# Optimization experiments

Measured on AMD Instinct MI355X. Metric: run time of the kernel, lower is better.

## Reference

```python
import jax, jax.numpy as jnp
import numpy as np


def setup_inputs() -> dict:
    key = jax.random.key(0)
    ks = jax.random.split(key, 5)
    B, C, H, W = 16, 512, 64, 64
    cm = cn = C // 4  # int(C*0.5*0.5)
    # kaiming_normal fan_out for 1x1 conv: std = sqrt(2 / out_channels)
    def kaiming(k, out_c, in_c):
        return jax.random.normal(k, (out_c, in_c), jnp.float32) * np.sqrt(2.0 / out_c)
    return {
        "x": jax.random.normal(ks[0], (B, C, H, W), jnp.float32),
        "WA": kaiming(ks[1], cm, C), "bA": jnp.zeros((cm,), jnp.float32),
        "WB": kaiming(ks[2], cn, C), "bB": jnp.zeros((cn,), jnp.float32),
        "WV": kaiming(ks[3], cn, C), "bV": jnp.zeros((cn,), jnp.float32),
        "WR": kaiming(ks[4], C, cm), "bR": jnp.zeros((C,), jnp.float32),
    }


def reference(x, WA, bA, WB, bB, WV, bV, WR, bR):
    b, c, h, w = x.shape
    n = h * w
    xf = x.reshape(b, c, n)  # [b, c, n] flattened spatial
    # 1x1 convs == per-pixel GEMMs
    A = jnp.einsum('mc,bcn->bmn', WA, xf) + bA[None, :, None]          # [b, cm, n]
    Bm = jax.nn.softmax(jnp.einsum('mc,bcn->bmn', WB, xf) + bB[None, :, None], axis=1)  # softmax over channels
    Vm = jax.nn.softmax(jnp.einsum('mc,bcn->bmn', WV, xf) + bV[None, :, None], axis=1)
    # second-order pooling: global descriptors [b, cm, cn]
    gd = jnp.einsum('bmn,bkn->bmk', A, Bm)
    # distribute: [b, cm, n]
    Z = jnp.einsum('bmk,bkn->bmn', gd, Vm)
    # reconstruct 1x1 conv back to c channels
    out = jnp.einsum('cm,bmn->bcn', WR, Z) + bR[None, :, None]
    return out.reshape(b, c, h, w)
```

## Files before the change

### kernel.cpp

```cpp
#include <hip/hip_runtime.h>
#include <hip/hip_fp16.h>


typedef _Float16 half8 __attribute__((ext_vector_type(8)));
typedef float f32x4 __attribute__((ext_vector_type(4)));

__device__ __forceinline__ unsigned short f2h(float v) {
  return __builtin_bit_cast(unsigned short, (_Float16)v);
}

__device__ __forceinline__ f32x4 mfma16(half8 a, half8 b, f32x4 c) {
  return __builtin_amdgcn_mfma_f32_16x16x32_f16(a, b, c, 0, 0, 0);
}

__device__ __forceinline__ int perm32(int v) {
  return (((v & 15) >> 2) << 3) | (((v >> 4) & 1) << 2) | (v & 3);
}

__device__ __forceinline__ void glds16(const unsigned short* g, unsigned short* l) {
  __builtin_amdgcn_global_load_lds(
      (const __attribute__((address_space(1))) unsigned int*)g,
      (__attribute__((address_space(3))) unsigned int*)l, 16, 0, 0);
}

__device__ __forceinline__ void stage_glds(unsigned short* lds,
                                           const unsigned short* g,
                                           int gs, int k0) {
  const int lane = threadIdx.x & 63;
  const int w = threadIdx.x >> 6;
#pragma unroll
  for (int p = 0; p < 2; ++p) {
    int g0 = (w + p * 4) * 64;
    int gi = g0 + lane;
    int row = gi & 127, kg = gi >> 7;
    glds16(g + (size_t)row * gs + k0 + kg * 8, lds + g0 * 8);
  }
}

__device__ __forceinline__ half8 ld_frag(const unsigned short* lds, int row) {
  int kg = (threadIdx.x & 63) >> 4;
  uint4 u = *(const uint4*)&lds[(kg * 128 + row) * 8];
  return __builtin_bit_cast(half8, u);
}

__global__ __launch_bounds__(256) void k_prep_w(
    const float* __restrict__ WA, const float* __restrict__ WB,
    const float* __restrict__ WV, const float* __restrict__ WR,
    unsigned short* __restrict__ Wh, unsigned short* __restrict__ WRh) {
  int idx = blockIdx.x * 256 + threadIdx.x;
  if (idx < 196608) {
    int mg = idx >> 16, r = idx & 65535;
    const float* src = (mg == 0) ? WA : ((mg == 1) ? WB : WV);
    Wh[(idx & ~31) | perm32(idx & 31)] = f2h(src[r]);
  } else {
    int r = idx - 196608;
    WRh[(r & ~31) | perm32(r & 31)] = f2h(WR[r]);
  }
}

__global__ __launch_bounds__(256) void k_transpose_x(
    const float* __restrict__ x, unsigned short* __restrict__ xT) {
  const int n0 = blockIdx.x * 64, c0 = blockIdx.y * 64, b = blockIdx.z;
  __shared__ float sT[64][65];
  const int t = threadIdx.x;
  const int tr = t >> 4, tc4 = (t & 15) * 4;
#pragma unroll
  for (int i = 0; i < 4; ++i) {
    int c = tr + i * 16;
    float4 v = *(const float4*)&x[((size_t)b * 512 + c0 + c) * 4096 + n0 + tc4];
    sT[c][tc4 + 0] = v.x; sT[c][tc4 + 1] = v.y;
    sT[c][tc4 + 2] = v.z; sT[c][tc4 + 3] = v.w;
  }
  __syncthreads();
#pragma unroll
  for (int i = 0; i < 4; ++i) {
    int n = tr + i * 16;
    int cq = tc4;
    ushort4 o;
    o.x = f2h(sT[cq + 0][n]); o.y = f2h(sT[cq + 1][n]);
    o.z = f2h(sT[cq + 2][n]); o.w = f2h(sT[cq + 3][n]);
    int cperm = c0 + (cq & ~31) + perm32(cq & 31);
    *(ushort4*)&xT[((size_t)b * 4096 + n0 + n) * 512 + cperm] = o;
  }
}

__global__ __launch_bounds__(256) void k_gemm_abv(
    const unsigned short* __restrict__ xT, const unsigned short* __restrict__ Wh,
    const float* __restrict__ bA, const float* __restrict__ bB,
    const float* __restrict__ bV,
    unsigned short* __restrict__ Aout, unsigned short* __restrict__ Bmout,
    unsigned short* __restrict__ VmTout) {
  const int nt = blockIdx.x, mg = blockIdx.y, b = blockIdx.z;
  const int tid = threadIdx.x, lane = tid & 63;
  const int w = tid >> 6, wr = w >> 1, wc = w & 1;
  const int kg = lane >> 4, lidx = lane & 15;

  __shared__ unsigned short sW[4096], sX[4096];
  __shared__ float colmax[2][128], colsum[2][128], sBias[128];

  const float* bias = (mg == 0) ? bA : ((mg == 1) ? bB : bV);
  if (tid < 128) sBias[tid] = bias[tid];

  const unsigned short* Wg = Wh + (size_t)mg * 128 * 512;
  const unsigned short* Xg = xT + ((size_t)b * 4096 + (size_t)nt * 128) * 512;

  f32x4 acc[4][4];
#pragma unroll
  for (int mf = 0; mf < 4; ++mf)
#pragma unroll
    for (int nf = 0; nf < 4; ++nf) acc[mf][nf] = (f32x4){0.f, 0.f, 0.f, 0.f};

  for (int k0 = 0; k0 < 512; k0 += 32) {
    stage_glds(sW, Wg, 512, k0);
    stage_glds(sX, Xg, 512, k0);
    __syncthreads();
    half8 af[4];
#pragma unroll
    for (int mf = 0; mf < 4; ++mf) af[mf] = ld_frag(sW, wr * 64 + mf * 16 + lidx);
#pragma unroll
    for (int nf = 0; nf < 4; ++nf) {
      half8 bf = ld_frag(sX, wc * 64 + nf * 16 + lidx);
#pragma unroll
      for (int mf = 0; mf < 4; ++mf) acc[mf][nf] = mfma16(af[mf], bf, acc[mf][nf]);
    }
    __syncthreads();
  }

#pragma unroll
  for (int mf = 0; mf < 4; ++mf)
#pragma unroll
    for (int i = 0; i < 4; ++i) {
      float bb = sBias[wr * 64 + mf * 16 + kg * 4 + i];
#pragma unroll
      for (int nf = 0; nf < 4; ++nf) acc[mf][nf][i] += bb;
    }

  int npg[4];
#pragma unroll
  for (int nf = 0; nf < 4; ++nf) {
    int nin = nf * 16 + lidx;
    npg[nf] = nt * 128 + wc * 64 + (nin & ~31) + perm32(nin & 31);
  }

  const size_t bofs = (size_t)b * 128 * 4096;
  if (mg == 0) {
#pragma unroll
    for (int mf = 0; mf < 4; ++mf)
#pragma unroll
      for (int nf = 0; nf < 4; ++nf)
#pragma unroll
        for (int i = 0; i < 4; ++i) {
          int m_ = wr * 64 + mf * 16 + kg * 4 + i;
          Aout[bofs + (size_t)m_ * 4096 + npg[nf]] = f2h(acc[mf][nf][i]);
        }
    return;
  }

  float cmax[4], csum[4];
#pragma unroll
  for (int nf = 0; nf < 4; ++nf) {
    float m = -1e30f;
#pragma unroll
    for (int mf = 0; mf < 4; ++mf)
#pragma unroll
      for (int i = 0; i < 4; ++i) m = fmaxf(m, acc[mf][nf][i]);
    m = fmaxf(m, __shfl_xor(m, 16));
    m = fmaxf(m, __shfl_xor(m, 32));
    cmax[nf] = m;
  }
  if (kg == 0) {
#pragma unroll
    for (int nf = 0; nf < 4; ++nf) colmax[wr][wc * 64 + nf * 16 + lidx] = cmax[nf];
  }
  __syncthreads();
#pragma unroll
  for (int nf = 0; nf < 4; ++nf)
    cmax[nf] = fmaxf(cmax[nf], colmax[wr ^ 1][wc * 64 + nf * 16 + lidx]);
#pragma unroll
  for (int nf = 0; nf < 4; ++nf) {
    float s = 0.f;
#pragma unroll
    for (int mf = 0; mf < 4; ++mf)
#pragma unroll
      for (int i = 0; i < 4; ++i) {
        float e = __expf(acc[mf][nf][i] - cmax[nf]);
        acc[mf][nf][i] = e;
        s += e;
      }
    s += __shfl_xor(s, 16);
    s += __shfl_xor(s, 32);
    csum[nf] = s;
  }
  if (kg == 0) {
#pragma unroll
    for (int nf = 0; nf < 4; ++nf) colsum[wr][wc * 64 + nf * 16 + lidx] = csum[nf];
  }
  __syncthreads();
  float inv_s[4];
#pragma unroll
  for (int nf = 0; nf < 4; ++nf)
    inv_s[nf] = 1.f / (csum[nf] + colsum[wr ^ 1][wc * 64 + nf * 16 + lidx]);

  if (mg == 1) {
#pragma unroll
    for (int mf = 0; mf < 4; ++mf)
#pragma unroll
      for (int nf = 0; nf < 4; ++nf)
#pragma unroll
        for (int i = 0; i < 4; ++i) {
          int m_ = wr * 64 + mf * 16 + kg * 4 + i;
          Bmout[bofs + (size_t)m_ * 4096 + npg[nf]] = f2h(acc[mf][nf][i] * inv_s[nf]);
        }
  } else {
    const size_t vofs = (size_t)b * 4096 * 128;
#pragma unroll
    for (int mf = 0; mf < 4; ++mf)
#pragma unroll
      for (int nf = 0; nf < 4; ++nf) {
        int m0 = wr * 64 + mf * 16 + kg * 4;
        int mp = (m0 & ~31) + perm32(m0 & 31);
        int n_ = nt * 128 + wc * 64 + nf * 16 + lidx;
        ushort4 pk;
        pk.x = f2h(acc[mf][nf][0] * inv_s[nf]);
        pk.y = f2h(acc[mf][nf][1] * inv_s[nf]);
        pk.z = f2h(acc[mf][nf][2] * inv_s[nf]);
        pk.w = f2h(acc[mf][nf][3] * inv_s[nf]);
        *(ushort4*)&VmTout[vofs + (size_t)n_ * 128 + mp] = pk;
      }
  }
}

__global__ __launch_bounds__(256) void k_gd(
    const unsigned short* __restrict__ A, const unsigned short* __restrict__ Bm,
    float* __restrict__ gd) {
  const int ks = blockIdx.x, b = blockIdx.y;
  const int tid = threadIdx.x, lane = tid & 63;
  const int w = tid >> 6, wr = w >> 1, wc = w & 1;
  const int kg = lane >> 4, lidx = lane & 15;
  __shared__ unsigned short sA[4096], sB[4096];
  const unsigned short* Ab = A + (size_t)b * 128 * 4096 + (size_t)ks * 256;
  const unsigned short* Bb = Bm + (size_t)b * 128 * 4096 + (size_t)ks * 256;

  f32x4 acc[4][4];
#pragma unroll
  for (int mf = 0; mf < 4; ++mf)
#pragma unroll
    for (int nf = 0; nf < 4; ++nf) acc[mf][nf] = (f32x4){0.f, 0.f, 0.f, 0.f};

  for (int k0 = 0; k0 < 256; k0 += 32) {
    stage_glds(sA, Ab, 4096, k0);
    stage_glds(sB, Bb, 4096, k0);
    __syncthreads();
    half8 af[4];
#pragma unroll
    for (int mf = 0; mf < 4; ++mf) af[mf] = ld_frag(sA, wr * 64 + mf * 16 + lidx);
#pragma unroll
    for (int nf = 0; nf < 4; ++nf) {
      half8 bf = ld_frag(sB, wc * 64 + nf * 16 + lidx);
#pragma unroll
      for (int mf = 0; mf < 4; ++mf) acc[mf][nf] = mfma16(af[mf], bf, acc[mf][nf]);
    }
    __syncthreads();
  }
  float* gb = gd + (size_t)b * 128 * 128;
#pragma unroll
  for (int mf = 0; mf < 4; ++mf)
#pragma unroll
    for (int nf = 0; nf < 4; ++nf)
#pragma unroll
      for (int i = 0; i < 4; ++i) {
        int m_ = wr * 64 + mf * 16 + kg * 4 + i;
        int k2 = wc * 64 + nf * 16 + lidx;
        atomicAdd(&gb[(size_t)m_ * 128 + k2], acc[mf][nf][i]);
      }
}

__global__ __launch_bounds__(256) void k_z(
    const float* __restrict__ gd, const unsigned short* __restrict__ VmT,
    unsigned short* __restrict__ ZT) {
  const int nt = blockIdx.x, b = blockIdx.y;
  const int tid = threadIdx.x, lane = tid & 63;
  const int w = tid >> 6, wr = w >> 1, wc = w & 1;
  const int kg = lane >> 4, lidx = lane & 15;
  __shared__ unsigned short sG[4096], sV[4096];
  const float4* gb = (const float4*)(gd + (size_t)b * 128 * 128);
  const unsigned short* Vb = VmT + ((size_t)b * 4096 + (size_t)nt * 128) * 128;

  f32x4 acc[4][4];
#pragma unroll
  for (int mf = 0; mf < 4; ++mf)
#pragma unroll
    for (int nf = 0; nf < 4; ++nf) acc[mf][nf] = (f32x4){0.f, 0.f, 0.f, 0.f};

  for (int k0 = 0; k0 < 128; k0 += 32) {
#pragma unroll
    for (int i = 0; i < 4; ++i) {
      int c = tid + 256 * i;
      int row = c >> 3, q8 = c & 7;
      float4 v = gb[row * 32 + (k0 >> 2) + q8];
      unsigned int lo = (unsigned)f2h(v.x) | ((unsigned)f2h(v.y) << 16);
      unsigned int hi = (unsigned)f2h(v.z) | ((unsigned)f2h(v.w) << 16);
      int kgq = q8 & 3, h = q8 >> 2;
      *(uint2*)&sG[(kgq * 128 + row) * 8 + h * 4] = make_uint2(lo, hi);
    }
    stage_glds(sV, Vb, 128, k0);
    __syncthreads();
    half8 af[4];
#pragma unroll
    for (int mf = 0; mf < 4; ++mf) af[mf] = ld_frag(sG, wr * 64 + mf * 16 + lidx);
#pragma unroll
    for (int nf = 0; nf < 4; ++nf) {
      half8 bf = ld_frag(sV, wc * 64 + nf * 16 + lidx);
#pragma unroll
      for (int mf = 0; mf < 4; ++mf) acc[mf][nf] = mfma16(af[mf], bf, acc[mf][nf]);
    }
    __syncthreads();
  }
  const size_t zofs = (size_t)b * 4096 * 128;
#pragma unroll
  for (int mf = 0; mf < 4; ++mf)
#pragma unroll
    for (int nf = 0; nf < 4; ++nf) {
      int m0 = wr * 64 + mf * 16 + kg * 4;
      int mp = (m0 & ~31) + perm32(m0 & 31);
      int n_ = nt * 128 + wc * 64 + nf * 16 + lidx;
      ushort4 pk;
      pk.x = f2h(acc[mf][nf][0]);
      pk.y = f2h(acc[mf][nf][1]);
      pk.z = f2h(acc[mf][nf][2]);
      pk.w = f2h(acc[mf][nf][3]);
      *(ushort4*)&ZT[zofs + (size_t)n_ * 128 + mp] = pk;
    }
}

__global__ __launch_bounds__(256) void k_out(
    const unsigned short* __restrict__ WRh, const unsigned short* __restrict__ ZT,
    const float* __restrict__ bR, float* __restrict__ out) {
  const int nt = blockIdx.x, ct = blockIdx.y, b = blockIdx.z;
  const int tid = threadIdx.x, lane = tid & 63;
  const int w = tid >> 6, wr = w >> 1, wc = w & 1;
  const int kg = lane >> 4, lidx = lane & 15;
  __shared__ unsigned short sW[4096], sZ[4096];
  __shared__ float sBias[128];
  if (tid < 128) sBias[tid] = bR[ct * 128 + tid];
  const unsigned short* Wb = WRh + (size_t)ct * 128 * 128;
  const unsigned short* Zb = ZT + ((size_t)b * 4096 + (size_t)nt * 128) * 128;

  f32x4 acc[4][4];
#pragma unroll
  for (int mf = 0; mf < 4; ++mf)
#pragma unroll
    for (int nf = 0; nf < 4; ++nf) acc[mf][nf] = (f32x4){0.f, 0.f, 0.f, 0.f};

  for (int k0 = 0; k0 < 128; k0 += 32) {
    stage_glds(sW, Wb, 128, k0);
    stage_glds(sZ, Zb, 128, k0);
    __syncthreads();
    half8 af[4];
#pragma unroll
    for (int mf = 0; mf < 4; ++mf) af[mf] = ld_frag(sW, wr * 64 + mf * 16 + lidx);
#pragma unroll
    for (int nf = 0; nf < 4; ++nf) {
      half8 bf = ld_frag(sZ, wc * 64 + nf * 16 + lidx);
#pragma unroll
      for (int mf = 0; mf < 4; ++mf) acc[mf][nf] = mfma16(af[mf], bf, acc[mf][nf]);
    }
    __syncthreads();
  }
#pragma unroll
  for (int mf = 0; mf < 4; ++mf)
#pragma unroll
    for (int nf = 0; nf < 4; ++nf)
#pragma unroll
      for (int i = 0; i < 4; ++i) {
        int cl = wr * 64 + mf * 16 + kg * 4 + i;
        int n_ = nt * 128 + wc * 64 + nf * 16 + lidx;
        out[((size_t)b * 512 + ct * 128 + cl) * 4096 + n_] = acc[mf][nf][i] + sBias[cl];
      }
}

extern "C" void kernel_launch(void* const* d_in, const int* in_sizes, int n_in,
                              void* d_out, int out_size, void* d_ws, size_t ws_size,
                              hipStream_t stream) {
  const float* x  = (const float*)d_in[0];
  const float* WA = (const float*)d_in[1];
  const float* bA = (const float*)d_in[2];
  const float* WB = (const float*)d_in[3];
  const float* bB = (const float*)d_in[4];
  const float* WV = (const float*)d_in[5];
  const float* bV = (const float*)d_in[6];
  const float* WR = (const float*)d_in[7];
  const float* bR = (const float*)d_in[8];
  float* out = (float*)d_out;

  char* ws = (char*)d_ws;
  unsigned short* Wh   = (unsigned short*)(ws);
  unsigned short* WRh  = (unsigned short*)(ws + 393216);
  unsigned short* xT   = (unsigned short*)(ws + 524288);
  unsigned short* Aout = (unsigned short*)(ws + 67633152);
  unsigned short* Bm   = (unsigned short*)(ws + 84410368);
  unsigned short* VmT  = (unsigned short*)(ws + 101187584);
  float*          gd   = (float*)(ws + 117964800);
  unsigned short* ZT   = (unsigned short*)(ws + 119013376);

  hipMemsetAsync(gd, 0, (size_t)16 * 128 * 128 * sizeof(float), stream);
  k_prep_w<<<1024, 256, 0, stream>>>(WA, WB, WV, WR, Wh, WRh);
  k_transpose_x<<<dim3(64, 8, 16), 256, 0, stream>>>(x, xT);
  k_gemm_abv<<<dim3(32, 3, 16), 256, 0, stream>>>(xT, Wh, bA, bB, bV, Aout, Bm, VmT);
  k_gd<<<dim3(16, 16), 256, 0, stream>>>(Aout, Bm, gd);
  k_z<<<dim3(32, 16), 256, 0, stream>>>(gd, VmT, ZT);
  k_out<<<dim3(32, 4, 16), 256, 0, stream>>>(WRh, ZT, bR, out);
}
```

Before: 184.0 us.

## Fuse x transpose, ABV GEMM and gd pooling; fold WR into gd

Removes the separate fp32→fp16 transpose of x: the fused kernel reads x directly, converts it in registers and double-buffers x and W tiles in shared memory. All three projections (A, Bm, Vm) are computed in one 384-thread block. A and Bm stay in LDS and their per-tile contribution to gd is accumulated with atomics, so the large A/Bm intermediates are never written to global memory. Reassociation multiplies WR by gd per batch (k_gw), which removes the Z pass and lets k_out consume Vm directly. The trade-offs are fewer blocks (512) with heavy LDS use, and an added fp16 rounding on the combined WR·gd weights.

```diff
diff --git a/kernel.cpp b/kernel.cpp
--- a/kernel.cpp
+++ b/kernel.cpp
@@ -8,24 +8,29 @@
 __device__ __forceinline__ unsigned short f2h(float v) {
   return __builtin_bit_cast(unsigned short, (_Float16)v);
 }
-
+__device__ __forceinline__ unsigned pk2(float a, float b) {
+  return (unsigned)f2h(a) | ((unsigned)f2h(b) << 16);
+}
 __device__ __forceinline__ f32x4 mfma16(half8 a, half8 b, f32x4 c) {
   return __builtin_amdgcn_mfma_f32_16x16x32_f16(a, b, c, 0, 0, 0);
 }
-
 __device__ __forceinline__ int perm32(int v) {
   return (((v & 15) >> 2) << 3) | (((v >> 4) & 1) << 2) | (v & 3);
 }
-
 __device__ __forceinline__ void glds16(const unsigned short* g, unsigned short* l) {
   __builtin_amdgcn_global_load_lds(
       (const __attribute__((address_space(1))) unsigned int*)g,
       (__attribute__((address_space(3))) unsigned int*)l, 16, 0, 0);
 }
-
-__device__ __forceinline__ void stage_glds(unsigned short* lds,
-                                           const unsigned short* g,
-                                           int gs, int k0) {
+__device__ __forceinline__ half8 ld_frag(const unsigned short* lds, int row) {
+  int kg = (threadIdx.x & 63) >> 4;
+  uint4 u = *(const uint4*)&lds[(kg * 128 + row) * 8];
+  return __builtin_bit_cast(half8, u);
+}
+
+__device__ __forceinline__ void stage_glds256(unsigned short* lds,
+                                              const unsigned short* g,
+                                              int gs, int k0) {
   const int lane = threadIdx.x & 63;
   const int w = threadIdx.x >> 6;
 #pragma unroll
@@ -37,209 +42,246 @@
   }
 }
 
-__device__ __forceinline__ half8 ld_frag(const unsigned short* lds, int row) {
-  int kg = (threadIdx.x & 63) >> 4;
-  uint4 u = *(const uint4*)&lds[(kg * 128 + row) * 8];
-  return __builtin_bit_cast(half8, u);
-}
-
-__global__ __launch_bounds__(256) void k_prep_w(
+__global__ __launch_bounds__(256) void k_prep(
     const float* __restrict__ WA, const float* __restrict__ WB,
     const float* __restrict__ WV, const float* __restrict__ WR,
-    unsigned short* __restrict__ Wh, unsigned short* __restrict__ WRh) {
+    unsigned short* __restrict__ Wh, unsigned short* __restrict__ WRh,
+    float* __restrict__ gdT) {
   int idx = blockIdx.x * 256 + threadIdx.x;
   if (idx < 196608) {
     int mg = idx >> 16, r = idx & 65535;
     const float* src = (mg == 0) ? WA : ((mg == 1) ? WB : WV);
     Wh[(idx & ~31) | perm32(idx & 31)] = f2h(src[r]);
-  } else {
+  } else if (idx < 262144) {
     int r = idx - 196608;
     WRh[(r & ~31) | perm32(r & 31)] = f2h(WR[r]);
-  }
-}
-
-__global__ __launch_bounds__(256) void k_transpose_x(
-    const float* __restrict__ x, unsigned short* __restrict__ xT) {
-  const int n0 = blockIdx.x * 64, c0 = blockIdx.y * 64, b = blockIdx.z;
-  __shared__ float sT[64][65];
-  const int t = threadIdx.x;
-  const int tr = t >> 4, tc4 = (t & 15) * 4;
-#pragma unroll
-  for (int i = 0; i < 4; ++i) {
-    int c = tr + i * 16;
-    float4 v = *(const float4*)&x[((size_t)b * 512 + c0 + c) * 4096 + n0 + tc4];
-    sT[c][tc4 + 0] = v.x; sT[c][tc4 + 1] = v.y;
-    sT[c][tc4 + 2] = v.z; sT[c][tc4 + 3] = v.w;
-  }
-  __syncthreads();
-#pragma unroll
-  for (int i = 0; i < 4; ++i) {
-    int n = tr + i * 16;
-    int cq = tc4;
-    ushort4 o;
-    o.x = f2h(sT[cq + 0][n]); o.y = f2h(sT[cq + 1][n]);
-    o.z = f2h(sT[cq + 2][n]); o.w = f2h(sT[cq + 3][n]);
-    int cperm = c0 + (cq & ~31) + perm32(cq & 31);
-    *(ushort4*)&xT[((size_t)b * 4096 + n0 + n) * 512 + cperm] = o;
-  }
-}
-
-__global__ __launch_bounds__(256) void k_gemm_abv(
-    const unsigned short* __restrict__ xT, const unsigned short* __restrict__ Wh,
+  } else {
+    gdT[idx - 262144] = 0.f;
+  }
+}
+
+__global__ __launch_bounds__(384) void k_abv_gd(
+    const float* __restrict__ x, const unsigned short* __restrict__ Wh,
     const float* __restrict__ bA, const float* __restrict__ bB,
     const float* __restrict__ bV,
-    unsigned short* __restrict__ Aout, unsigned short* __restrict__ Bmout,
-    unsigned short* __restrict__ VmTout) {
-  const int nt = blockIdx.x, mg = blockIdx.y, b = blockIdx.z;
-  const int tid = threadIdx.x, lane = tid & 63;
-  const int w = tid >> 6, wr = w >> 1, wc = w & 1;
+    unsigned short* __restrict__ VmT, float* __restrict__ gdT) {
+  const int nt = blockIdx.x, b = blockIdx.y;
+  const int tid = threadIdx.x, lane = tid & 63, w = tid >> 6;
   const int kg = lane >> 4, lidx = lane & 15;
-
-  __shared__ unsigned short sW[4096], sX[4096];
-  __shared__ float colmax[2][128], colsum[2][128], sBias[128];
-
-  const float* bias = (mg == 0) ? bA : ((mg == 1) ? bB : bV);
-  if (tid < 128) sBias[tid] = bias[tid];
-
-  const unsigned short* Wg = Wh + (size_t)mg * 128 * 512;
-  const unsigned short* Xg = xT + ((size_t)b * 4096 + (size_t)nt * 128) * 512;
-
-  f32x4 acc[4][4];
+  const int mg = w >> 1, wh = w & 1;
+
+  __shared__ unsigned short smem[32768];
+  __shared__ float cmaxs[2][2][128], csums[2][2][128];
+  __shared__ float sBias[384];
+
+  sBias[tid] = ((mg == 0) ? bA : ((mg == 1) ? bB : bV))[tid & 127];
+
+  const float* xbase = x + (size_t)b * 512 * 4096 + nt * 128;
+  const int xn = tid & 127;
+  const int xkg = tid >> 7;
+  const bool x2 = (tid >= 256);
+
+  float xr[16];
+
+#define XLOAD(K0) do { \
+  _Pragma("unroll") for (int j = 0; j < 4; ++j) { \
+    xr[j]     = xbase[(size_t)((K0) + 4 * xkg + j) * 4096 + xn]; \
+    xr[4 + j] = xbase[(size_t)((K0) + 16 + 4 * xkg + j) * 4096 + xn]; \
+  } \
+  if (x2) { _Pragma("unroll") for (int j = 0; j < 4; ++j) { \
+    xr[8 + j]  = xbase[(size_t)((K0) + 12 + j) * 4096 + xn]; \
+    xr[12 + j] = xbase[(size_t)((K0) + 28 + j) * 4096 + xn]; \
+  } } } while (0)
+
+#define XWRITE(SX) do { \
+  uint4 u_; \
+  u_.x = pk2(xr[0], xr[1]); u_.y = pk2(xr[2], xr[3]); \
+  u_.z = pk2(xr[4], xr[5]); u_.w = pk2(xr[6], xr[7]); \
+  *(uint4*)&(SX)[(xkg * 128 + xn) * 8] = u_; \
+  if (x2) { \
+    uint4 v_; \
+    v_.x = pk2(xr[8], xr[9]);   v_.y = pk2(xr[10], xr[11]); \
+    v_.z = pk2(xr[12], xr[13]); v_.w = pk2(xr[14], xr[15]); \
+    *(uint4*)&(SX)[(3 * 128 + xn) * 8] = v_; \
+  } } while (0)
+
+#define WSTAGE(SW, K0) do { \
+  _Pragma("unroll") for (int p = 0; p < 4; ++p) { \
+    int g0_ = (w * 4 + p) * 64; \
+    int gi_ = g0_ + lane; \
+    int mgt_ = gi_ >> 9, q_ = gi_ & 511; \
+    int kgw_ = q_ >> 7, row_ = q_ & 127; \
+    glds16(Wh + mgt_ * 65536 + row_ * 512 + (K0) + kgw_ * 8, (SW) + g0_ * 8); \
+  } } while (0)
+
+  f32x4 acc[4][8];
 #pragma unroll
   for (int mf = 0; mf < 4; ++mf)
 #pragma unroll
-    for (int nf = 0; nf < 4; ++nf) acc[mf][nf] = (f32x4){0.f, 0.f, 0.f, 0.f};
-
-  for (int k0 = 0; k0 < 512; k0 += 32) {
-    stage_glds(sW, Wg, 512, k0);
-    stage_glds(sX, Xg, 512, k0);
+    for (int nf = 0; nf < 8; ++nf) acc[mf][nf] = (f32x4){0.f, 0.f, 0.f, 0.f};
+
+  XLOAD(0);
+  WSTAGE(smem, 0);
+  XWRITE(smem + 12288);
+
+  for (int ks = 0; ks < 16; ++ks) {
+    unsigned short* cw = smem + (ks & 1) * 16384;
+    unsigned short* nx = smem + ((ks & 1) ^ 1) * 16384;
     __syncthreads();
+    if (ks < 15) {
+      XLOAD((ks + 1) * 32);
+      WSTAGE(nx, (ks + 1) * 32);
+    }
     half8 af[4];
 #pragma unroll
-    for (int mf = 0; mf < 4; ++mf) af[mf] = ld_frag(sW, wr * 64 + mf * 16 + lidx);
-#pragma unroll
-    for (int nf = 0; nf < 4; ++nf) {
-      half8 bf = ld_frag(sX, wc * 64 + nf * 16 + lidx);
-#pragma unroll
-      for (int mf = 0; mf < 4; ++mf) acc[mf][nf] = mfma16(af[mf], bf, acc[mf][nf]);
-    }
-    __syncthreads();
+    for (int mf = 0; mf < 4; ++mf)
+      af[mf] = ld_frag(cw + mg * 4096, wh * 64 + mf * 16 + lidx);
+#pragma unroll
+    for (int nf = 0; nf < 8; ++nf) {
+      half8 bf = ld_frag(cw + 12288, nf * 16 + lidx);
+#pragma unroll
+      for (int mf = 0; mf < 4; ++mf)
+        acc[mf][nf] = mfma16(af[mf], bf, acc[mf][nf]);
+    }
+    if (ks < 15) XWRITE(nx + 12288);
   }
 
 #pragma unroll
   for (int mf = 0; mf < 4; ++mf)
 #pragma unroll
     for (int i = 0; i < 4; ++i) {
-      float bb = sBias[wr * 64 + mf * 16 + kg * 4 + i];
-#pragma unroll
-      for (int nf = 0; nf < 4; ++nf) acc[mf][nf][i] += bb;
-    }
-
-  int npg[4];
-#pragma unroll
-  for (int nf = 0; nf < 4; ++nf) {
-    int nin = nf * 16 + lidx;
-    npg[nf] = nt * 128 + wc * 64 + (nin & ~31) + perm32(nin & 31);
-  }
-
-  const size_t bofs = (size_t)b * 128 * 4096;
-  if (mg == 0) {
+      float bb = sBias[mg * 128 + wh * 64 + mf * 16 + kg * 4 + i];
+#pragma unroll
+      for (int nf = 0; nf < 8; ++nf) acc[mf][nf][i] += bb;
+    }
+
+  float inv_s[8];
+  if (mg) {
+#pragma unroll
+    for (int nf = 0; nf < 8; ++nf) {
+      float m = -1e30f;
+#pragma unroll
+      for (int mf = 0; mf < 4; ++mf)
+#pragma unroll
+        for (int i = 0; i < 4; ++i) m = fmaxf(m, acc[mf][nf][i]);
+      m = fmaxf(m, __shfl_xor(m, 16));
+      m = fmaxf(m, __shfl_xor(m, 32));
+      if (kg == 0) cmaxs[mg - 1][wh][nf * 16 + lidx] = m;
+      inv_s[nf] = m;
+    }
+  }
+  __syncthreads();
+  if (mg) {
+#pragma unroll
+    for (int nf = 0; nf < 8; ++nf) {
+      float m = fmaxf(inv_s[nf], cmaxs[mg - 1][wh ^ 1][nf * 16 + lidx]);
+      float s = 0.f;
+#pragma unroll
+      for (int mf = 0; mf < 4; ++mf)
+#pragma unroll
+        for (int i = 0; i < 4; ++i) {
+          float e = __expf(acc[mf][nf][i] - m);
+          acc[mf][nf][i] = e;
+          s += e;
+        }
+      s += __shfl_xor(s, 16);
+      s += __shfl_xor(s, 32);
+      if (kg == 0) csums[mg - 1][wh][nf * 16 + lidx] = s;
+      inv_s[nf] = s;
+    }
+  }
+  __syncthreads();
+  if (mg) {
+#pragma unroll
+    for (int nf = 0; nf < 8; ++nf)
+      inv_s[nf] = 1.f / (inv_s[nf] + csums[mg - 1][wh ^ 1][nf * 16 + lidx]);
+  }
+
+  unsigned short* sA2 = smem;
+  unsigned short* sB2 = smem + 16384;
+
+  if (mg != 2) {
+    unsigned short* dst = (mg == 0) ? sA2 : sB2;
+#pragma unroll
+    for (int nf = 0; nf < 8; ++nf) {
+      int base = (nf >> 1) * 4096 + (lidx >> 2) * 1024 + (nf & 1) * 4 + (lidx & 3);
+#pragma unroll
+      for (int mf = 0; mf < 4; ++mf)
+#pragma unroll
+        for (int i = 0; i < 4; ++i) {
+          int m_ = wh * 64 + mf * 16 + kg * 4 + i;
+          float v = acc[mf][nf][i];
+          dst[base + m_ * 8] = f2h(mg ? v * inv_s[nf] : v);
+        }
+    }
+  }
+  __syncthreads();
+
+  if (mg != 2) {
+    const int gr = wh, gc = mg;
+    f32x4 g2[4][4];
 #pragma unroll
     for (int mf = 0; mf < 4; ++mf)
 #pragma unroll
+      for (int nf = 0; nf < 4; ++nf) g2[mf][nf] = (f32x4){0.f, 0.f, 0.f, 0.f};
+#pragma unroll
+    for (int ks2 = 0; ks2 < 4; ++ks2) {
+      half8 af2[4];
+#pragma unroll
+      for (int mf = 0; mf < 4; ++mf)
+        af2[mf] = ld_frag(sA2 + ks2 * 4096, gr * 64 + mf * 16 + lidx);
+#pragma unroll
+      for (int nf = 0; nf < 4; ++nf) {
+        half8 bf2 = ld_frag(sB2 + ks2 * 4096, gc * 64 + nf * 16 + lidx);
+#pragma unroll
+        for (int mf = 0; mf < 4; ++mf)
+          g2[mf][nf] = mfma16(af2[mf], bf2, g2[mf][nf]);
+      }
+    }
+    float* gb = gdT + (size_t)b * 16384;
+#pragma unroll
+    for (int mf = 0; mf < 4; ++mf)
+#pragma unroll
       for (int nf = 0; nf < 4; ++nf)
 #pragma unroll
         for (int i = 0; i < 4; ++i) {
-          int m_ = wr * 64 + mf * 16 + kg * 4 + i;
-          Aout[bofs + (size_t)m_ * 4096 + npg[nf]] = f2h(acc[mf][nf][i]);
-        }
-    return;
-  }
-
-  float cmax[4], csum[4];
-#pragma unroll
-  for (int nf = 0; nf < 4; ++nf) {
-    float m = -1e30f;
-#pragma unroll
-    for (int mf = 0; mf < 4; ++mf)
-#pragma unroll
-      for (int i = 0; i < 4; ++i) m = fmaxf(m, acc[mf][nf][i]);
-    m = fmaxf(m, __shfl_xor(m, 16));
-    m = fmaxf(m, __shfl_xor(m, 32));
-    cmax[nf] = m;
-  }
-  if (kg == 0) {
-#pragma unroll
-    for (int nf = 0; nf < 4; ++nf) colmax[wr][wc * 64 + nf * 16 + lidx] = cmax[nf];
-  }
-  __syncthreads();
-#pragma unroll
-  for (int nf = 0; nf < 4; ++nf)
-    cmax[nf] = fmaxf(cmax[nf], colmax[wr ^ 1][wc * 64 + nf * 16 + lidx]);
-#pragma unroll
-  for (int nf = 0; nf < 4; ++nf) {
-    float s = 0.f;
-#pragma unroll
-    for (int mf = 0; mf < 4; ++mf)
-#pragma unroll
-      for (int i = 0; i < 4; ++i) {
-        float e = __expf(acc[mf][nf][i] - cmax[nf]);
-        acc[mf][nf][i] = e;
-        s += e;
-      }
-    s += __shfl_xor(s, 16);
-    s += __shfl_xor(s, 32);
-    csum[nf] = s;
-  }
-  if (kg == 0) {
-#pragma unroll
-    for (int nf = 0; nf < 4; ++nf) colsum[wr][wc * 64 + nf * 16 + lidx] = csum[nf];
-  }
-  __syncthreads();
-  float inv_s[4];
-#pragma unroll
-  for (int nf = 0; nf < 4; ++nf)
-    inv_s[nf] = 1.f / (csum[nf] + colsum[wr ^ 1][wc * 64 + nf * 16 + lidx]);
-
-  if (mg == 1) {
-#pragma unroll
-    for (int mf = 0; mf < 4; ++mf)
-#pragma unroll
-      for (int nf = 0; nf < 4; ++nf)
-#pragma unroll
-        for (int i = 0; i < 4; ++i) {
-          int m_ = wr * 64 + mf * 16 + kg * 4 + i;
-          Bmout[bofs + (size_t)m_ * 4096 + npg[nf]] = f2h(acc[mf][nf][i] * inv_s[nf]);
+          int m_ = gr * 64 + mf * 16 + kg * 4 + i;
+          int k2 = gc * 64 + nf * 16 + lidx;
+          atomicAdd(&gb[k2 * 128 + m_], g2[mf][nf][i]);
         }
   } else {
-    const size_t vofs = (size_t)b * 4096 * 128;
-#pragma unroll
-    for (int mf = 0; mf < 4; ++mf)
-#pragma unroll
-      for (int nf = 0; nf < 4; ++nf) {
-        int m0 = wr * 64 + mf * 16 + kg * 4;
-        int mp = (m0 & ~31) + perm32(m0 & 31);
-        int n_ = nt * 128 + wc * 64 + nf * 16 + lidx;
+    const size_t vofs = ((size_t)b * 4096 + (size_t)nt * 128) * 128;
+#pragma unroll
+    for (int mf = 0; mf < 4; ++mf) {
+      int m0 = wh * 64 + mf * 16 + kg * 4;
+      int mp = (m0 & ~31) + perm32(m0 & 31);
+#pragma unroll
+      for (int nf = 0; nf < 8; ++nf) {
+        int n_ = nf * 16 + lidx;
         ushort4 pk;
         pk.x = f2h(acc[mf][nf][0] * inv_s[nf]);
         pk.y = f2h(acc[mf][nf][1] * inv_s[nf]);
         pk.z = f2h(acc[mf][nf][2] * inv_s[nf]);
         pk.w = f2h(acc[mf][nf][3] * inv_s[nf]);
-        *(ushort4*)&VmTout[vofs + (size_t)n_ * 128 + mp] = pk;
+        *(ushort4*)&VmT[vofs + (size_t)n_ * 128 + mp] = pk;
       }
-  }
-}
-
-__global__ __launch_bounds__(256) void k_gd(
-    const unsigned short* __restrict__ A, const unsigned short* __restrict__ Bm,
-    float* __restrict__ gd) {
-  const int ks = blockIdx.x, b = blockIdx.y;
+    }
+  }
+#undef XLOAD
+#undef XWRITE
+#undef WSTAGE
+}
+
+__global__ __launch_bounds__(256) void k_gw(
+    const float* __restrict__ gdT, const unsigned short* __restrict__ WRh,
+    unsigned short* __restrict__ GWh) {
+  const int ct = blockIdx.x, b = blockIdx.y;
   const int tid = threadIdx.x, lane = tid & 63;
   const int w = tid >> 6, wr = w >> 1, wc = w & 1;
   const int kg = lane >> 4, lidx = lane & 15;
-  __shared__ unsigned short sA[4096], sB[4096];
-  const unsigned short* Ab = A + (size_t)b * 128 * 4096 + (size_t)ks * 256;
-  const unsigned short* Bb = Bm + (size_t)b * 128 * 4096 + (size_t)ks * 256;
+  __shared__ unsigned short sG[4096], sWr[4096];
+  const float* gb = gdT + (size_t)b * 16384;
+  const unsigned short* Wb = WRh + ct * 128 * 128;
 
   f32x4 acc[4][4];
 #pragma unroll
@@ -247,94 +289,50 @@
 #pragma unroll
     for (int nf = 0; nf < 4; ++nf) acc[mf][nf] = (f32x4){0.f, 0.f, 0.f, 0.f};
 
-  for (int k0 = 0; k0 < 256; k0 += 32) {
-    stage_glds(sA, Ab, 4096, k0);
-    stage_glds(sB, Bb, 4096, k0);
+  for (int k0 = 0; k0 < 128; k0 += 32) {
+#pragma unroll
+    for (int p = 0; p < 2; ++p) {
+      int g = tid + p * 256;
+      int row = g & 127, kgx = g >> 7;
+      const float* s0 = &gb[row * 128 + k0 + 4 * kgx];
+      float4 v0 = *(const float4*)s0;
+      float4 v1 = *(const float4*)(s0 + 16);
+      uint4 u;
+      u.x = pk2(v0.x, v0.y); u.y = pk2(v0.z, v0.w);
+      u.z = pk2(v1.x, v1.y); u.w = pk2(v1.z, v1.w);
+      *(uint4*)&sG[g * 8] = u;
+    }
+    stage_glds256(sWr, Wb, 128, k0);
     __syncthreads();
     half8 af[4];
 #pragma unroll
-    for (int mf = 0; mf < 4; ++mf) af[mf] = ld_frag(sA, wr * 64 + mf * 16 + lidx);
+    for (int mf = 0; mf < 4; ++mf) af[mf] = ld_frag(sG, wr * 64 + mf * 16 + lidx);
 #pragma unroll
     for (int nf = 0; nf < 4; ++nf) {
-      half8 bf = ld_frag(sB, wc * 64 + nf * 16 + lidx);
+      half8 bf = ld_frag(sWr, wc * 64 + nf * 16 + lidx);
 #pragma unroll
       for (int mf = 0; mf < 4; ++mf) acc[mf][nf] = mfma16(af[mf], bf, acc[mf][nf]);
     }
     __syncthreads();
   }
-  float* gb = gd + (size_t)b * 128 * 128;
-#pragma unroll
-  for (int mf = 0; mf < 4; ++mf)
-#pragma unroll
-    for (int nf = 0; nf < 4; ++nf)
-#pragma unroll
-      for (int i = 0; i < 4; ++i) {
-        int m_ = wr * 64 + mf * 16 + kg * 4 + i;
-        int k2 = wc * 64 + nf * 16 + lidx;
-        atomicAdd(&gb[(size_t)m_ * 128 + k2], acc[mf][nf][i]);
-      }
-}
-
-__global__ __launch_bounds__(256) void k_z(
-    const float* __restrict__ gd, const unsigned short* __restrict__ VmT,
-    unsigned short* __restrict__ ZT) {
-  const int nt = blockIdx.x, b = blockIdx.y;
-  const int tid = threadIdx.x, lane = tid & 63;
-  const int w = tid >> 6, wr = w >> 1, wc = w & 1;
-  const int kg = lane >> 4, lidx = lane & 15;
-  __shared__ unsigned short sG[4096], sV[4096];
-  const float4* gb = (const float4*)(gd + (size_t)b * 128 * 128);
-  const unsigned short* Vb = VmT + ((size_t)b * 4096 + (size_t)nt * 128) * 128;
-
-  f32x4 acc[4][4];
-#pragma unroll
-  for (int mf = 0; mf < 4; ++mf)
-#pragma unroll
-    for (int nf = 0; nf < 4; ++nf) acc[mf][nf] = (f32x4){0.f, 0.f, 0.f, 0.f};
-
-  for (int k0 = 0; k0 < 128; k0 += 32) {
-#pragma unroll
-    for (int i = 0; i < 4; ++i) {
-      int c = tid + 256 * i;
-      int row = c >> 3, q8 = c & 7;
-      float4 v = gb[row * 32 + (k0 >> 2) + q8];
-      unsigned int lo = (unsigned)f2h(v.x) | ((unsigned)f2h(v.y) << 16);
-      unsigned int hi = (unsigned)f2h(v.z) | ((unsigned)f2h(v.w) << 16);
-      int kgq = q8 & 3, h = q8 >> 2;
-      *(uint2*)&sG[(kgq * 128 + row) * 8 + h * 4] = make_uint2(lo, hi);
-    }
-    stage_glds(sV, Vb, 128, k0);
-    __syncthreads();
-    half8 af[4];
-#pragma unroll
-    for (int mf = 0; mf < 4; ++mf) af[mf] = ld_frag(sG, wr * 64 + mf * 16 + lidx);
+  const size_t gofs = ((size_t)b * 512 + (size_t)ct * 128) * 128;
+#pragma unroll
+  for (int mf = 0; mf < 4; ++mf) {
+    int k0g = wr * 64 + mf * 16 + kg * 4;
+    int kp = (k0g & ~31) + perm32(k0g & 31);
 #pragma unroll
     for (int nf = 0; nf < 4; ++nf) {
-      half8 bf = ld_frag(sV, wc * 64 + nf * 16 + lidx);
-#pragma unroll
-      for (int mf = 0; mf < 4; ++mf) acc[mf][nf] = mfma16(af[mf], bf, acc[mf][nf]);
-    }
-    __syncthreads();
-  }
-  const size_t zofs = (size_t)b * 4096 * 128;
-#pragma unroll
-  for (int mf = 0; mf < 4; ++mf)
-#pragma unroll
-    for (int nf = 0; nf < 4; ++nf) {
-      int m0 = wr * 64 + mf * 16 + kg * 4;
-      int mp = (m0 & ~31) + perm32(m0 & 31);
-      int n_ = nt * 128 + wc * 64 + nf * 16 + lidx;
+      int c_ = wc * 64 + nf * 16 + lidx;
       ushort4 pk;
-      pk.x = f2h(acc[mf][nf][0]);
-      pk.y = f2h(acc[mf][nf][1]);
-      pk.z = f2h(acc[mf][nf][2]);
-      pk.w = f2h(acc[mf][nf][3]);
-      *(ushort4*)&ZT[zofs + (size_t)n_ * 128 + mp] = pk;
-    }
+      pk.x = f2h(acc[mf][nf][0]); pk.y = f2h(acc[mf][nf][1]);
+      pk.z = f2h(acc[mf][nf][2]); pk.w = f2h(acc[mf][nf][3]);
+      *(ushort4*)&GWh[gofs + (size_t)c_ * 128 + kp] = pk;
+    }
+  }
 }
 
 __global__ __launch_bounds__(256) void k_out(
-    const unsigned short* __restrict__ WRh, const unsigned short* __restrict__ ZT,
+    const unsigned short* __restrict__ GWh, const unsigned short* __restrict__ VmT,
     const float* __restrict__ bR, float* __restrict__ out) {
   const int nt = blockIdx.x, ct = blockIdx.y, b = blockIdx.z;
   const int tid = threadIdx.x, lane = tid & 63;
@@ -343,8 +341,8 @@
   __shared__ unsigned short sW[4096], sZ[4096];
   __shared__ float sBias[128];
   if (tid < 128) sBias[tid] = bR[ct * 128 + tid];
-  const unsigned short* Wb = WRh + (size_t)ct * 128 * 128;
-  const unsigned short* Zb = ZT + ((size_t)b * 4096 + (size_t)nt * 128) * 128;
+  const unsigned short* Wb = GWh + ((size_t)b * 512 + (size_t)ct * 128) * 128;
+  const unsigned short* Zb = VmT + ((size_t)b * 4096 + (size_t)nt * 128) * 128;
 
   f32x4 acc[4][4];
 #pragma unroll
@@ -353,8 +351,8 @@
     for (int nf = 0; nf < 4; ++nf) acc[mf][nf] = (f32x4){0.f, 0.f, 0.f, 0.f};
 
   for (int k0 = 0; k0 < 128; k0 += 32) {
-    stage_glds(sW, Wb, 128, k0);
-    stage_glds(sZ, Zb, 128, k0);
+    stage_glds256(sW, Wb, 128, k0);
+    stage_glds256(sZ, Zb, 128, k0);
     __syncthreads();
     half8 af[4];
 #pragma unroll
@@ -394,20 +392,14 @@
   float* out = (float*)d_out;
 
   char* ws = (char*)d_ws;
-  unsigned short* Wh   = (unsigned short*)(ws);
-  unsigned short* WRh  = (unsigned short*)(ws + 393216);
-  unsigned short* xT   = (unsigned short*)(ws + 524288);
-  unsigned short* Aout = (unsigned short*)(ws + 67633152);
-  unsigned short* Bm   = (unsigned short*)(ws + 84410368);
-  unsigned short* VmT  = (unsigned short*)(ws + 101187584);
-  float*          gd   = (float*)(ws + 117964800);
-  unsigned short* ZT   = (unsigned short*)(ws + 119013376);
-
-  hipMemsetAsync(gd, 0, (size_t)16 * 128 * 128 * sizeof(float), stream);
-  k_prep_w<<<1024, 256, 0, stream>>>(WA, WB, WV, WR, Wh, WRh);
-  k_transpose_x<<<dim3(64, 8, 16), 256, 0, stream>>>(x, xT);
-  k_gemm_abv<<<dim3(32, 3, 16), 256, 0, stream>>>(xT, Wh, bA, bB, bV, Aout, Bm, VmT);
-  k_gd<<<dim3(16, 16), 256, 0, stream>>>(Aout, Bm, gd);
-  k_z<<<dim3(32, 16), 256, 0, stream>>>(gd, VmT, ZT);
-  k_out<<<dim3(32, 4, 16), 256, 0, stream>>>(WRh, ZT, bR, out);
-}
+  unsigned short* Wh  = (unsigned short*)(ws);
+  unsigned short* WRh = (unsigned short*)(ws + 393216);
+  unsigned short* VmT = (unsigned short*)(ws + 524288);
+  float*          gdT = (float*)(ws + 17301504);
+  unsigned short* GWh = (unsigned short*)(ws + 18350080);
+
+  k_prep<<<2048, 256, 0, stream>>>(WA, WB, WV, WR, Wh, WRh, gdT);
+  k_abv_gd<<<dim3(32, 16), 384, 0, stream>>>(x, Wh, bA, bB, bV, VmT, gdT);
+  k_gw<<<dim3(4, 16), 256, 0, stream>>>(gdT, WRh, GWh);
+  k_out<<<dim3(32, 4, 16), 256, 0, stream>>>(GWh, VmT, bR, out);
+}
```

New measurement: 245.9 us. 33.6% more time.

## Fold WR into per-batch gd weights and read fp32 x directly in GEMM

Applied to the files above, without the earlier changes.

Drops the separate x transpose/fp16 conversion kernel. The projection GEMM now stages fp32 x tiles into LDS with an XOR swizzle and converts to fp16 while building fragments. It also reassociates WR·(gd·Vm) into (WR·gd)·Vm, computing a small per-batch 512x128 weight (k_gw) so the Z intermediate and its GEMM over all pixels disappear. Block order is swapped so the three projection groups sharing an x tile run adjacently. The risks are doubled LDS traffic for fp32 x, scalar LDS gathers when building fragments, and fp16 rounding of the fused weight.

```diff
diff --git a/kernel.cpp b/kernel.cpp
--- a/kernel.cpp
+++ b/kernel.cpp
@@ -8,24 +8,45 @@
 __device__ __forceinline__ unsigned short f2h(float v) {
   return __builtin_bit_cast(unsigned short, (_Float16)v);
 }
-
+__device__ __forceinline__ unsigned pk2(float a, float b) {
+  return (unsigned)f2h(a) | ((unsigned)f2h(b) << 16);
+}
 __device__ __forceinline__ f32x4 mfma16(half8 a, half8 b, f32x4 c) {
   return __builtin_amdgcn_mfma_f32_16x16x32_f16(a, b, c, 0, 0, 0);
 }
-
 __device__ __forceinline__ int perm32(int v) {
   return (((v & 15) >> 2) << 3) | (((v >> 4) & 1) << 2) | (v & 3);
 }
-
-__device__ __forceinline__ void glds16(const unsigned short* g, unsigned short* l) {
+__device__ __forceinline__ void glds16(const void* g, void* l) {
   __builtin_amdgcn_global_load_lds(
       (const __attribute__((address_space(1))) unsigned int*)g,
       (__attribute__((address_space(3))) unsigned int*)l, 16, 0, 0);
 }
-
-__device__ __forceinline__ void stage_glds(unsigned short* lds,
-                                           const unsigned short* g,
-                                           int gs, int k0) {
+__device__ __forceinline__ half8 ld_frag(const unsigned short* lds, int row) {
+  int kg = (threadIdx.x & 63) >> 4;
+  uint4 u = *(const uint4*)&lds[(kg * 128 + row) * 8];
+  return __builtin_bit_cast(half8, u);
+}
+__device__ __forceinline__ half8 ld_frag_x128(const float* lds, int n) {
+  const int lane = threadIdx.x & 63;
+  const int kg = lane >> 4;
+  const int q = n >> 2, r = n & 3;
+  float v[8];
+#pragma unroll
+  for (int j = 0; j < 4; ++j) {
+    int c0 = 4 * kg + j, c1 = c0 + 16;
+    v[j]     = lds[c0 * 128 + ((q ^ c0) & 31) * 4 + r];
+    v[4 + j] = lds[c1 * 128 + ((q ^ c1) & 31) * 4 + r];
+  }
+  uint4 u;
+  u.x = pk2(v[0], v[1]); u.y = pk2(v[2], v[3]);
+  u.z = pk2(v[4], v[5]); u.w = pk2(v[6], v[7]);
+  return __builtin_bit_cast(half8, u);
+}
+
+__device__ __forceinline__ void stage_glds256(unsigned short* lds,
+                                              const unsigned short* g,
+                                              int gs, int k0) {
   const int lane = threadIdx.x & 63;
   const int w = threadIdx.x >> 6;
 #pragma unroll
@@ -37,13 +58,7 @@
   }
 }
 
-__device__ __forceinline__ half8 ld_frag(const unsigned short* lds, int row) {
-  int kg = (threadIdx.x & 63) >> 4;
-  uint4 u = *(const uint4*)&lds[(kg * 128 + row) * 8];
-  return __builtin_bit_cast(half8, u);
-}
-
-__global__ __launch_bounds__(256) void k_prep_w(
+__global__ __launch_bounds__(256) void k_prep(
     const float* __restrict__ WA, const float* __restrict__ WB,
     const float* __restrict__ WV, const float* __restrict__ WR,
     unsigned short* __restrict__ Wh, unsigned short* __restrict__ WRh) {
@@ -58,51 +73,35 @@
   }
 }
 
-__global__ __launch_bounds__(256) void k_transpose_x(
-    const float* __restrict__ x, unsigned short* __restrict__ xT) {
-  const int n0 = blockIdx.x * 64, c0 = blockIdx.y * 64, b = blockIdx.z;
-  __shared__ float sT[64][65];
-  const int t = threadIdx.x;
-  const int tr = t >> 4, tc4 = (t & 15) * 4;
-#pragma unroll
-  for (int i = 0; i < 4; ++i) {
-    int c = tr + i * 16;
-    float4 v = *(const float4*)&x[((size_t)b * 512 + c0 + c) * 4096 + n0 + tc4];
-    sT[c][tc4 + 0] = v.x; sT[c][tc4 + 1] = v.y;
-    sT[c][tc4 + 2] = v.z; sT[c][tc4 + 3] = v.w;
-  }
-  __syncthreads();
-#pragma unroll
-  for (int i = 0; i < 4; ++i) {
-    int n = tr + i * 16;
-    int cq = tc4;
-    ushort4 o;
-    o.x = f2h(sT[cq + 0][n]); o.y = f2h(sT[cq + 1][n]);
-    o.z = f2h(sT[cq + 2][n]); o.w = f2h(sT[cq + 3][n]);
-    int cperm = c0 + (cq & ~31) + perm32(cq & 31);
-    *(ushort4*)&xT[((size_t)b * 4096 + n0 + n) * 512 + cperm] = o;
-  }
-}
-
 __global__ __launch_bounds__(256) void k_gemm_abv(
-    const unsigned short* __restrict__ xT, const unsigned short* __restrict__ Wh,
+    const float* __restrict__ x, const unsigned short* __restrict__ Wh,
     const float* __restrict__ bA, const float* __restrict__ bB,
     const float* __restrict__ bV,
     unsigned short* __restrict__ Aout, unsigned short* __restrict__ Bmout,
     unsigned short* __restrict__ VmTout) {
-  const int nt = blockIdx.x, mg = blockIdx.y, b = blockIdx.z;
+  const int mg = blockIdx.x, nt = blockIdx.y, b = blockIdx.z;
   const int tid = threadIdx.x, lane = tid & 63;
   const int w = tid >> 6, wr = w >> 1, wc = w & 1;
   const int kg = lane >> 4, lidx = lane & 15;
 
-  __shared__ unsigned short sW[4096], sX[4096];
+  __shared__ unsigned short sW[4096];
+  __shared__ __align__(16) float sX[4096];
   __shared__ float colmax[2][128], colsum[2][128], sBias[128];
 
   const float* bias = (mg == 0) ? bA : ((mg == 1) ? bB : bV);
   if (tid < 128) sBias[tid] = bias[tid];
 
   const unsigned short* Wg = Wh + (size_t)mg * 128 * 512;
-  const unsigned short* Xg = xT + ((size_t)b * 4096 + (size_t)nt * 128) * 512;
+  const float* xsrc = x + (size_t)b * 512 * 4096 + nt * 128;
+
+#define XSTAGE32(K0) do { \
+  _Pragma("unroll") for (int p_ = 0; p_ < 4; ++p_) { \
+    int g0_ = (tid >> 6) * 64 + p_ * 256;    \
+    int s_ = g0_ + lane; \
+    int c_ = s_ >> 5, qp_ = s_ & 31; \
+    glds16(xsrc + (size_t)((K0) + c_) * 4096 + ((qp_ ^ c_) << 2), \
+           sX + (size_t)g0_ * 4); \
+  } } while (0)
 
   f32x4 acc[4][4];
 #pragma unroll
@@ -111,15 +110,15 @@
     for (int nf = 0; nf < 4; ++nf) acc[mf][nf] = (f32x4){0.f, 0.f, 0.f, 0.f};
 
   for (int k0 = 0; k0 < 512; k0 += 32) {
-    stage_glds(sW, Wg, 512, k0);
-    stage_glds(sX, Xg, 512, k0);
+    stage_glds256(sW, Wg, 512, k0);
+    XSTAGE32(k0);
     __syncthreads();
     half8 af[4];
 #pragma unroll
     for (int mf = 0; mf < 4; ++mf) af[mf] = ld_frag(sW, wr * 64 + mf * 16 + lidx);
 #pragma unroll
     for (int nf = 0; nf < 4; ++nf) {
-      half8 bf = ld_frag(sX, wc * 64 + nf * 16 + lidx);
+      half8 bf = ld_frag_x128(sX, wc * 64 + nf * 16 + lidx);
 #pragma unroll
       for (int mf = 0; mf < 4; ++mf) acc[mf][nf] = mfma16(af[mf], bf, acc[mf][nf]);
     }
@@ -228,11 +227,12 @@
         *(ushort4*)&VmTout[vofs + (size_t)n_ * 128 + mp] = pk;
       }
   }
+#undef XSTAGE32
 }
 
 __global__ __launch_bounds__(256) void k_gd(
     const unsigned short* __restrict__ A, const unsigned short* __restrict__ Bm,
-    float* __restrict__ gd) {
+    float* __restrict__ gdT) {
   const int ks = blockIdx.x, b = blockIdx.y;
   const int tid = threadIdx.x, lane = tid & 63;
   const int w = tid >> 6, wr = w >> 1, wc = w & 1;
@@ -248,8 +248,8 @@
     for (int nf = 0; nf < 4; ++nf) acc[mf][nf] = (f32x4){0.f, 0.f, 0.f, 0.f};
 
   for (int k0 = 0; k0 < 256; k0 += 32) {
-    stage_glds(sA, Ab, 4096, k0);
-    stage_glds(sB, Bb, 4096, k0);
+    stage_glds256(sA, Ab, 4096, k0);
+    stage_glds256(sB, Bb, 4096, k0);
     __syncthreads();
     half8 af[4];
 #pragma unroll
@@ -262,7 +262,7 @@
     }
     __syncthreads();
   }
-  float* gb = gd + (size_t)b * 128 * 128;
+  float* gb = gdT + (size_t)b * 128 * 128;
 #pragma unroll
   for (int mf = 0; mf < 4; ++mf)
 #pragma unroll
@@ -271,20 +271,20 @@
       for (int i = 0; i < 4; ++i) {
         int m_ = wr * 64 + mf * 16 + kg * 4 + i;
         int k2 = wc * 64 + nf * 16 + lidx;
-        atomicAdd(&gb[(size_t)m_ * 128 + k2], acc[mf][nf][i]);
+        atomicAdd(&gb[(size_t)k2 * 128 + m_], acc[mf][nf][i]);
       }
 }
 
-__global__ __launch_bounds__(256) void k_z(
-    const float* __restrict__ gd, const unsigned short* __restrict__ VmT,
-    unsigned short* __restrict__ ZT) {
-  const int nt = blockIdx.x, b = blockIdx.y;
+__global__ __launch_bounds__(256) void k_gw(
+    const float* __restrict__ gdT, const unsigned short* __restrict__ WRh,
+    unsigned short* __restrict__ GWh) {
+  const int ct = blockIdx.x, b = blockIdx.y;
   const int tid = threadIdx.x, lane = tid & 63;
   const int w = tid >> 6, wr = w >> 1, wc = w & 1;
   const int kg = lane >> 4, lidx = lane & 15;
-  __shared__ unsigned short sG[4096], sV[4096];
-  const float4* gb = (const float4*)(gd + (size_t)b * 128 * 128);
-  const unsigned short* Vb = VmT + ((size_t)b * 4096 + (size_t)nt * 128) * 128;
+  __shared__ unsigned short sG[4096], sWr[4096];
+  const float* gb = gdT + (size_t)b * 16384;
+  const unsigned short* Wb = WRh + ct * 128 * 128;
 
   f32x4 acc[4][4];
 #pragma unroll
@@ -294,47 +294,48 @@
 
   for (int k0 = 0; k0 < 128; k0 += 32) {
 #pragma unroll
-    for (int i = 0; i < 4; ++i) {
-      int c = tid + 256 * i;
-      int row = c >> 3, q8 = c & 7;
-      float4 v = gb[row * 32 + (k0 >> 2) + q8];
-      unsigned int lo = (unsigned)f2h(v.x) | ((unsigned)f2h(v.y) << 16);
-      unsigned int hi = (unsigned)f2h(v.z) | ((unsigned)f2h(v.w) << 16);
-      int kgq = q8 & 3, h = q8 >> 2;
-      *(uint2*)&sG[(kgq * 128 + row) * 8 + h * 4] = make_uint2(lo, hi);
-    }
-    stage_glds(sV, Vb, 128, k0);
+    for (int p = 0; p < 2; ++p) {
+      int g = tid + p * 256;
+      int row = g & 127, kgx = g >> 7;
+      const float* s0 = &gb[row * 128 + k0 + 4 * kgx];
+      float4 v0 = *(const float4*)s0;
+      float4 v1 = *(const float4*)(s0 + 16);
+      uint4 u;
+      u.x = pk2(v0.x, v0.y); u.y = pk2(v0.z, v0.w);
+      u.z = pk2(v1.x, v1.y); u.w = pk2(v1.z, v1.w);
+      *(uint4*)&sG[g * 8] = u;
+    }
+    stage_glds256(sWr, Wb, 128, k0);
     __syncthreads();
     half8 af[4];
 #pragma unroll
     for (int mf = 0; mf < 4; ++mf) af[mf] = ld_frag(sG, wr * 64 + mf * 16 + lidx);
 #pragma unroll
     for (int nf = 0; nf < 4; ++nf) {
-      half8 bf = ld_frag(sV, wc * 64 + nf * 16 + lidx);
+      half8 bf = ld_frag(sWr, wc * 64 + nf * 16 + lidx);
 #pragma unroll
       for (int mf = 0; mf < 4; ++mf) acc[mf][nf] = mfma16(af[mf], bf, acc[mf][nf]);
     }
     __syncthreads();
   }
-  const size_t zofs = (size_t)b * 4096 * 128;
-#pragma unroll
-  for (int mf = 0; mf < 4; ++mf)
+  const size_t gofs = ((size_t)b * 512 + (size_t)ct * 128) * 128;
+#pragma unroll
+  for (int mf = 0; mf < 4; ++mf) {
+    int k0g = wr * 64 + mf * 16 + kg * 4;
+    int kp = (k0g & ~31) + perm32(k0g & 31);
 #pragma unroll
     for (int nf = 0; nf < 4; ++nf) {
-      int m0 = wr * 64 + mf * 16 + kg * 4;
-      int mp = (m0 & ~31) + perm32(m0 & 31);
-      int n_ = nt * 128 + wc * 64 + nf * 16 + lidx;
+      int c_ = wc * 64 + nf * 16 + lidx;
       ushort4 pk;
-      pk.x = f2h(acc[mf][nf][0]);
-      pk.y = f2h(acc[mf][nf][1]);
-      pk.z = f2h(acc[mf][nf][2]);
-      pk.w = f2h(acc[mf][nf][3]);
-      *(ushort4*)&ZT[zofs + (size_t)n_ * 128 + mp] = pk;
-    }
+      pk.x = f2h(acc[mf][nf][0]); pk.y = f2h(acc[mf][nf][1]);
+      pk.z = f2h(acc[mf][nf][2]); pk.w = f2h(acc[mf][nf][3]);
+      *(ushort4*)&GWh[gofs + (size_t)c_ * 128 + kp] = pk;
+    }
+  }
 }
 
 __global__ __launch_bounds__(256) void k_out(
-    const unsigned short* __restrict__ WRh, const unsigned short* __restrict__ ZT,
+    const unsigned short* __restrict__ GWh, const unsigned short* __restrict__ VmT,
     const float* __restrict__ bR, float* __restrict__ out) {
   const int nt = blockIdx.x, ct = blockIdx.y, b = blockIdx.z;
   const int tid = threadIdx.x, lane = tid & 63;
@@ -343,8 +344,8 @@
   __shared__ unsigned short sW[4096], sZ[4096];
   __shared__ float sBias[128];
   if (tid < 128) sBias[tid] = bR[ct * 128 + tid];
-  const unsigned short* Wb = WRh + (size_t)ct * 128 * 128;
-  const unsigned short* Zb = ZT + ((size_t)b * 4096 + (size_t)nt * 128) * 128;
+  const unsigned short* Wb = GWh + ((size_t)b * 512 + (size_t)ct * 128) * 128;
+  const unsigned short* Zb = VmT + ((size_t)b * 4096 + (size_t)nt * 128) * 128;
 
   f32x4 acc[4][4];
 #pragma unroll
@@ -353,8 +354,8 @@
     for (int nf = 0; nf < 4; ++nf) acc[mf][nf] = (f32x4){0.f, 0.f, 0.f, 0.f};
 
   for (int k0 = 0; k0 < 128; k0 += 32) {
-    stage_glds(sW, Wb, 128, k0);
-    stage_glds(sZ, Zb, 128, k0);
+    stage_glds256(sW, Wb, 128, k0);
+    stage_glds256(sZ, Zb, 128, k0);
     __syncthreads();
     half8 af[4];
 #pragma unroll
@@ -394,20 +395,18 @@
   float* out = (float*)d_out;
 
   char* ws = (char*)d_ws;
-  unsigned short* Wh   = (unsigned short*)(ws);
-  unsigned short* WRh  = (unsigned short*)(ws + 393216);
-  unsigned short* xT   = (unsigned short*)(ws + 524288);
-  unsigned short* Aout = (unsigned short*)(ws + 67633152);
-  unsigned short* Bm   = (unsigned short*)(ws + 84410368);
-  unsigned short* VmT  = (unsigned short*)(ws + 101187584);
-  float*          gd   = (float*)(ws + 117964800);
-  unsigned short* ZT   = (unsigned short*)(ws + 119013376);
-
-  hipMemsetAsync(gd, 0, (size_t)16 * 128 * 128 * sizeof(float), stream);
-  k_prep_w<<<1024, 256, 0, stream>>>(WA, WB, WV, WR, Wh, WRh);
-  k_transpose_x<<<dim3(64, 8, 16), 256, 0, stream>>>(x, xT);
-  k_gemm_abv<<<dim3(32, 3, 16), 256, 0, stream>>>(xT, Wh, bA, bB, bV, Aout, Bm, VmT);
-  k_gd<<<dim3(16, 16), 256, 0, stream>>>(Aout, Bm, gd);
-  k_z<<<dim3(32, 16), 256, 0, stream>>>(gd, VmT, ZT);
-  k_out<<<dim3(32, 4, 16), 256, 0, stream>>>(WRh, ZT, bR, out);
-}
+  unsigned short* Wh  = (unsigned short*)(ws);
+  unsigned short* WRh = (unsigned short*)(ws + 393216);
+  unsigned short* A   = (unsigned short*)(ws + 524288);
+  unsigned short* Bm  = (unsigned short*)(ws + 17301504);
+  unsigned short* VmT = (unsigned short*)(ws + 34078720);
+  float*          gdT = (float*)(ws + 50855936);
+  unsigned short* GWh = (unsigned short*)(ws + 51904512);
+
+  hipMemsetAsync(gdT, 0, (size_t)16 * 128 * 128 * sizeof(float), stream);
+  k_prep<<<1024, 256, 0, stream>>>(WA, WB, WV, WR, Wh, WRh);
+  k_gemm_abv<<<dim3(3, 32, 16), 256, 0, stream>>>(x, Wh, bA, bB, bV, A, Bm, VmT);
+  k_gd<<<dim3(16, 16), 256, 0, stream>>>(A, Bm, gdT);
+  k_gw<<<dim3(4, 16), 256, 0, stream>>>(gdT, WRh, GWh);
+  k_out<<<dim3(32, 4, 16), 256, 0, stream>>>(GWh, VmT, bR, out);
+}
```

Measured after the change: 198.3 us. 1.08x slower.
